# Optimization experiments

Hardware: AMD Instinct MI355X
Metric: run time of the kernel (lower is better)

## Reference

```python
import jax, jax.numpy as jnp
import numpy as np

B, C, S, D = 64, 729, 243, 512


def _layer_norm(x, gamma, beta, eps=1e-5):
    mu = jnp.mean(x, axis=-1, keepdims=True)
    var = jnp.mean((x - mu) ** 2, axis=-1, keepdims=True)
    return (x - mu) * jax.lax.rsqrt(var + eps) * gamma + beta


def setup_inputs() -> dict:
    key = jax.random.key(0)
    ks = jax.random.split(key, 8)
    s = 1.0 / np.sqrt(D)
    return {
        "cand_feat": jax.random.normal(ks[0], (B, C, D), dtype=jnp.float32),
        "set_feat": jax.random.normal(ks[1], (B, S, D), dtype=jnp.float32),
        "W_vc": jax.random.uniform(ks[2], (D, D), jnp.float32, -s, s),
        "b_vc": jnp.zeros((D,), jnp.float32),
        "W_vs": jax.random.uniform(ks[3], (D, D), jnp.float32, -s, s),
        "b_vs": jnp.zeros((D,), jnp.float32),
        "ff_W1": jax.random.uniform(ks[4], (2 * D, D), jnp.float32, -s, s),
        "ff_b1": jnp.zeros((2 * D,), jnp.float32),
        "ff_W2": jax.random.uniform(ks[5], (D, 2 * D), jnp.float32, -1.0 / np.sqrt(2 * D), 1.0 / np.sqrt(2 * D)),
        "ff_b2": jnp.zeros((D,), jnp.float32),
        "g_set": jnp.ones((D,), jnp.float32),
        "be_set": jnp.zeros((D,), jnp.float32),
        "g_cand": jnp.ones((D,), jnp.float32),
        "be_cand": jnp.zeros((D,), jnp.float32),
        "g_ff": jnp.ones((D,), jnp.float32),
        "be_ff": jnp.zeros((D,), jnp.float32),
        "cand_to_set_idx": jax.random.randint(ks[6], (C, 3), 0, S, dtype=jnp.int64 if jax.config.jax_enable_x64 else jnp.int32),
    }


def reference(cand_feat, set_feat, W_vc, b_vc, W_vs, b_vs, ff_W1, ff_b1, ff_W2, ff_b2,
              g_set, be_set, g_cand, be_cand, g_ff, be_ff, cand_to_set_idx):
    b, c, d = cand_feat.shape
    idx = cand_to_set_idx.reshape(-1)  # (2187,)

    cand_msgs = cand_feat @ W_vc.T + b_vc              # (B, 729, D)
    msgs3 = jnp.repeat(cand_msgs, 3, axis=1)           # (B, 2187, D)
    set_updates = jnp.zeros_like(set_feat).at[:, idx, :].add(msgs3) / 9.0
    set_out = _layer_norm(set_feat + set_updates, g_set, be_set)

    # set -> cand: gather 3 sets per candidate, mean, linear
    gathered = set_out[:, idx, :].reshape(b, c, 3, d)  # (B, 729, 3, D)
    cand_updates = gathered.mean(axis=2) @ W_vs.T + b_vs
    cand_h = _layer_norm(cand_feat + cand_updates, g_cand, be_cand)

    # FF block with residual
    ff = jax.nn.relu(cand_h @ ff_W1.T + ff_b1) @ ff_W2.T + ff_b2
    cand_out = _layer_norm(cand_h + ff, g_ff, be_ff)
    return (cand_out, set_out)
```

## Files before the change

### kernel.cpp

```cpp
#include <hip/hip_runtime.h>

using u16 = unsigned short;
using u32 = unsigned int;

typedef __attribute__((ext_vector_type(8))) short bf16x8;
typedef __attribute__((ext_vector_type(4))) float f32x4;
typedef __attribute__((ext_vector_type(8))) u16 u16x8;
typedef __attribute__((ext_vector_type(4))) u16 u16x4;

constexpr int NB = 64, NC = 729, NS = 243, ND = 512, ND2 = 1024;
constexpr int MS = NB * NS;
constexpr int MC = NB * NC;

__device__ __forceinline__ u16 f2bf(float f) {
  u32 u = __builtin_bit_cast(u32, f);
  return (u16)((u + 0x7fffu + ((u >> 16) & 1u)) >> 16);
}
__device__ __forceinline__ float bf2f(u16 h) {
  return __builtin_bit_cast(float, (u32)h << 16);
}
__device__ __forceinline__ void gload16(const void* g, void* l) {
  __builtin_amdgcn_global_load_lds((const __attribute__((address_space(1))) u32*)g,
                                   (__attribute__((address_space(3))) u32*)l, 16, 0, 0);
}

__global__ __launch_bounds__(256) void cast_all_k(const float* __restrict__ s0,
                                                  const float* __restrict__ s1,
                                                  const float* __restrict__ s2,
                                                  const float* __restrict__ s3,
                                                  u16* __restrict__ d0, u16* __restrict__ d1,
                                                  u16* __restrict__ d2, u16* __restrict__ d3) {
  int i = blockIdx.x * 256 + threadIdx.x;
  const float* s; u16* d; int off;
  if (i < 65536)       { s = s0; d = d0; off = i; }
  else if (i < 131072) { s = s1; d = d1; off = i - 65536; }
  else if (i < 262144) { s = s2; d = d2; off = i - 131072; }
  else                 { s = s3; d = d3; off = i - 262144; }
  f32x4 v = ((const f32x4*)s)[off];
  u16x4 o;
  o.x = f2bf(v.x); o.y = f2bf(v.y); o.z = f2bf(v.z); o.w = f2bf(v.w);
  ((u16x4*)d)[off] = o;
}

__global__ __launch_bounds__(1024) void build_csr_k(const int* __restrict__ idx,
                                                    int* __restrict__ offs,
                                                    int* __restrict__ list) {
  constexpr int NE = 3 * NC;
  constexpr int NCH = (NE + 63) / 64;
  __shared__ int sidx[NE];
  __shared__ int lrank[NE];
  __shared__ int hist[NCH][NS];
  __shared__ int scan[256];
  __shared__ int soffs[NS];
  const int t = threadIdx.x;
  const int wv = t >> 6, ln = t & 63;

  for (int e = t; e < NE; e += 1024) sidx[e] = idx[e];
  for (int i = t; i < NCH * NS; i += 1024) (&hist[0][0])[i] = 0;
  __syncthreads();

  for (int c = wv; c < NCH; c += 16) {
    int e = c * 64 + ln;
    int s = (e < NE) ? sidx[e] : -1;
    int rank = 0, tot = 0;
#pragma unroll
    for (int l2 = 0; l2 < 64; ++l2) {
      int v = __shfl(s, l2);
      bool m = (v == s) && (s >= 0);
      rank += (m && (l2 < ln)) ? 1 : 0;
      tot  += m ? 1 : 0;
    }
    if (e < NE) {
      lrank[e] = rank;
      if (rank == 0) hist[c][s] = tot;
    }
  }
  __syncthreads();

  int mycnt = 0;
  if (t < NS) {
    int run = 0;
#pragma unroll 5
    for (int c = 0; c < NCH; ++c) { int v = hist[c][t]; hist[c][t] = run; run += v; }
    mycnt = run;
  }
  if (t < 256) scan[t] = (t < NS) ? mycnt : 0;
  __syncthreads();

  for (int d = 1; d < 256; d <<= 1) {
    int v = 0;
    if (t < 256 && t >= d) v = scan[t - d];
    __syncthreads();
    if (t < 256) scan[t] += v;
    __syncthreads();
  }
  if (t < NS) {
    soffs[t] = scan[t] - mycnt;
    offs[t] = scan[t] - mycnt;
  }
  if (t == 0) offs[NS] = NE;
  __syncthreads();

  for (int e = t; e < NE; e += 1024) {
    int s = sidx[e];
    list[soffs[s] + hist[e >> 6][s] + lrank[e]] = e / 3;
  }
}

__global__ __launch_bounds__(256) void agg_k(const float* __restrict__ cand_feat,
                                             const int* __restrict__ offs,
                                             const int* __restrict__ list,
                                             u16* __restrict__ agg) {
  int row = blockIdx.x * 4 + (threadIdx.x >> 6);
  if (row >= MS) return;
  int lane = threadIdx.x & 63;
  int b = row / NS, s = row - b * NS;
  int e0 = offs[s], e1 = offs[s + 1];
  const float* base = cand_feat + (size_t)b * NC * ND + lane * 8;
  f32x4 a0 = {0.f, 0.f, 0.f, 0.f}, a1 = {0.f, 0.f, 0.f, 0.f};
  for (int e = e0; e < e1; ++e) {
    const float* p = base + (size_t)list[e] * ND;
    a0 += *(const f32x4*)p;
    a1 += *(const f32x4*)(p + 4);
  }
  u16x8 o;
  o[0] = f2bf(a0.x); o[1] = f2bf(a0.y); o[2] = f2bf(a0.z); o[3] = f2bf(a0.w);
  o[4] = f2bf(a1.x); o[5] = f2bf(a1.y); o[6] = f2bf(a1.z); o[7] = f2bf(a1.w);
  *(u16x8*)(agg + (size_t)row * ND + lane * 8) = o;
}

template <int EP>
__global__ __launch_bounds__(256, 4) void gemm_k64(const u16* __restrict__ A,
                                                   const u16* __restrict__ Bw,
                                                   void* __restrict__ Out,
                                                   const float* __restrict__ bias,
                                                   int M, int N, int K) {
  constexpr int BK = 64;
  __shared__ u16 lA[128 * BK];
  __shared__ u16 lB[128 * BK];
  const int t = threadIdx.x, wid = t >> 6, lane = t & 63;
  const int NT = N >> 7;
  const int nwg = gridDim.x;
  int wg;
  { int q = nwg >> 3, r = nwg & 7, x = blockIdx.x & 7, p = blockIdx.x >> 3;
    wg = (x < r ? x * (q + 1) : r * (q + 1) + (x - r) * q) + p; }
  const int mt = wg / NT, nt = wg % NT;
  const int m0 = mt << 7, n0 = nt << 7;

  const u16* gA[4]; const u16* gB[4]; int ldo[4];
#pragma unroll
  for (int i = 0; i < 4; ++i) {
    int s = i * 256 + t;
    int r = s >> 3, j = s & 7;
    int cj = (j ^ (r & 7)) * 8;
    int ar = m0 + r; if (ar > M - 1) ar = M - 1;
    gA[i] = A + (size_t)ar * K + cj;
    gB[i] = Bw + (size_t)(n0 + r) * K + cj;
    ldo[i] = s * 8;
  }

  const int li = lane & 15, g0 = lane >> 4;
  const int wr = wid >> 1, wc = wid & 1;
  int aOff[4], bOff[4];
#pragma unroll
  for (int i = 0; i < 4; ++i) {
    int rowA = wr * 64 + i * 16 + li;
    int rowB = wc * 64 + i * 16 + li;
    aOff[i] = rowA * 64 + ((g0 ^ (li & 7)) << 3);
    bOff[i] = rowB * 64 + ((g0 ^ (li & 7)) << 3);
  }

  f32x4 acc[4][4] = {};

  for (int kt = 0; kt < K; kt += BK) {
#pragma unroll
    for (int i = 0; i < 4; ++i) gload16(gA[i], lA + ldo[i]);
#pragma unroll
    for (int i = 0; i < 4; ++i) gload16(gB[i], lB + ldo[i]);
#pragma unroll
    for (int i = 0; i < 4; ++i) { gA[i] += BK; gB[i] += BK; }
    __syncthreads();
#pragma unroll
    for (int kk = 0; kk < 2; ++kk) {
      bf16x8 af[4], bfr[4];
#pragma unroll
      for (int i = 0; i < 4; ++i) {
        af[i]  = *(const bf16x8*)(lA + (aOff[i] ^ (kk << 5)));
        bfr[i] = *(const bf16x8*)(lB + (bOff[i] ^ (kk << 5)));
      }
#pragma unroll
      for (int mi = 0; mi < 4; ++mi)
#pragma unroll
        for (int ni = 0; ni < 4; ++ni)
          acc[mi][ni] = __builtin_amdgcn_mfma_f32_16x16x32_bf16(af[mi], bfr[ni], acc[mi][ni], 0, 0, 0);
    }
    __syncthreads();
  }

  const int rb = m0 + wr * 64 + (g0 << 2);
  const int cb = n0 + wc * 64 + li;
  if (EP == 0) {
    float* O = (float*)Out;
#pragma unroll
    for (int mi = 0; mi < 4; ++mi)
#pragma unroll
      for (int ni = 0; ni < 4; ++ni) {
        int cc = cb + ni * 16;
#pragma unroll
        for (int r = 0; r < 4; ++r) {
          int rr = rb + mi * 16 + r;
          if (rr < M) O[(size_t)rr * N + cc] = acc[mi][ni][r];
        }
      }
  } else {
    u16* O = (u16*)Out;
    float bv[4];
#pragma unroll
    for (int ni = 0; ni < 4; ++ni) bv[ni] = (EP == 3) ? 0.0f : bias[cb + ni * 16];
#pragma unroll
    for (int mi = 0; mi < 4; ++mi)
#pragma unroll
      for (int ni = 0; ni < 4; ++ni) {
        int cc = cb + ni * 16;
#pragma unroll
        for (int r = 0; r < 4; ++r) {
          int rr = rb + mi * 16 + r;
          float v = acc[mi][ni][r] + bv[ni];
          if (EP == 1) v = fmaxf(v, 0.0f);
          if (rr < M) O[(size_t)rr * N + cc] = f2bf(v);
        }
      }
  }
}

__global__ __launch_bounds__(256) void set_ln_k(const u16* __restrict__ u1,
                                                const float* __restrict__ set_feat,
                                                const int* __restrict__ offs,
                                                const float* __restrict__ b_vc,
                                                const float* __restrict__ gam,
                                                const float* __restrict__ bet,
                                                float* __restrict__ set_out,
                                                u16* __restrict__ set_out_bf) {
  int row = blockIdx.x * 4 + (threadIdx.x >> 6);
  if (row >= MS) return;
  int lane = threadIdx.x & 63;
  int s = row % NS;
  float c9 = (float)(offs[s + 1] - offs[s]) * (1.0f / 9.0f);
  size_t base = (size_t)row * ND + lane * 8;
  u16x8 ua = *(const u16x8*)(u1 + base);
  f32x4 s0 = *(const f32x4*)(set_feat + base), s1  = *(const f32x4*)(set_feat + base + 4);
  f32x4 b0 = *(const f32x4*)(b_vc + lane * 8), b1  = *(const f32x4*)(b_vc + lane * 8 + 4);
  f32x4 x0, x1;
#pragma unroll
  for (int i = 0; i < 4; ++i) {
    x0[i] = s0[i] + bf2f(ua[i]) * (1.0f / 9.0f) + b0[i] * c9;
    x1[i] = s1[i] + bf2f(ua[i + 4]) * (1.0f / 9.0f) + b1[i] * c9;
  }
  float sm = 0.f, sq = 0.f;
#pragma unroll
  for (int i = 0; i < 4; ++i) { sm += x0[i] + x1[i]; sq += x0[i] * x0[i] + x1[i] * x1[i]; }
#pragma unroll
  for (int m = 32; m; m >>= 1) { sm += __shfl_xor(sm, m); sq += __shfl_xor(sq, m); }
  float mu = sm * (1.0f / ND);
  float rs = rsqrtf(sq * (1.0f / ND) - mu * mu + 1e-5f);
  f32x4 g0 = *(const f32x4*)(gam + lane * 8), g1 = *(const f32x4*)(gam + lane * 8 + 4);
  f32x4 e0 = *(const f32x4*)(bet + lane * 8), e1 = *(const f32x4*)(bet + lane * 8 + 4);
  f32x4 y0, y1; u16x8 ob;
#pragma unroll
  for (int i = 0; i < 4; ++i) {
    y0[i] = (x0[i] - mu) * rs * g0[i] + e0[i];
    y1[i] = (x1[i] - mu) * rs * g1[i] + e1[i];
    ob[i] = f2bf(y0[i]); ob[i + 4] = f2bf(y1[i]);
  }
  *(f32x4*)(set_out + base) = y0;
  *(f32x4*)(set_out + base + 4) = y1;
  *(u16x8*)(set_out_bf + base) = ob;
}

__global__ __launch_bounds__(256) void cand_ln_k(const float* __restrict__ cand_feat,
                                                 const u16* __restrict__ proj,
                                                 const int* __restrict__ cidx,
                                                 const float* __restrict__ b_vs,
                                                 const float* __restrict__ gam,
                                                 const float* __restrict__ bet,
                                                 u16* __restrict__ cand_h) {
  int row = blockIdx.x * 4 + (threadIdx.x >> 6);
  if (row >= MC) return;
  int lane = threadIdx.x & 63;
  int b = row / NC, c = row - b * NC;
  int i0 = cidx[c * 3], i1 = cidx[c * 3 + 1], i2 = cidx[c * 3 + 2];
  const u16* pb = proj + (size_t)b * NS * ND + lane * 8;
  u16x8 p0 = *(const u16x8*)(pb + (size_t)i0 * ND);
  u16x8 p1 = *(const u16x8*)(pb + (size_t)i1 * ND);
  u16x8 p2 = *(const u16x8*)(pb + (size_t)i2 * ND);
  size_t base = (size_t)row * ND + lane * 8;
  f32x4 c0 = *(const f32x4*)(cand_feat + base), c1 = *(const f32x4*)(cand_feat + base + 4);
  f32x4 v0 = *(const f32x4*)(b_vs + lane * 8),  v1 = *(const f32x4*)(b_vs + lane * 8 + 4);
  const float third = 1.0f / 3.0f;
  f32x4 x0, x1;
#pragma unroll
  for (int i = 0; i < 4; ++i) {
    x0[i] = c0[i] + (bf2f(p0[i]) + bf2f(p1[i]) + bf2f(p2[i])) * third + v0[i];
    x1[i] = c1[i] + (bf2f(p0[i + 4]) + bf2f(p1[i + 4]) + bf2f(p2[i + 4])) * third + v1[i];
  }
  float sm = 0.f, sq = 0.f;
#pragma unroll
  for (int i = 0; i < 4; ++i) { sm += x0[i] + x1[i]; sq += x0[i] * x0[i] + x1[i] * x1[i]; }
#pragma unroll
  for (int m = 32; m; m >>= 1) { sm += __shfl_xor(sm, m); sq += __shfl_xor(sq, m); }
  float mu = sm * (1.0f / ND);
  float rs = rsqrtf(sq * (1.0f / ND) - mu * mu + 1e-5f);
  f32x4 g0 = *(const f32x4*)(gam + lane * 8), g1 = *(const f32x4*)(gam + lane * 8 + 4);
  f32x4 e0 = *(const f32x4*)(bet + lane * 8), e1 = *(const f32x4*)(bet + lane * 8 + 4);
  u16x8 ob;
#pragma unroll
  for (int i = 0; i < 4; ++i) {
    ob[i]     = f2bf((x0[i] - mu) * rs * g0[i] + e0[i]);
    ob[i + 4] = f2bf((x1[i] - mu) * rs * g1[i] + e1[i]);
  }
  *(u16x8*)(cand_h + base) = ob;
}

__global__ __launch_bounds__(256) void ln_ff_k(const u16* __restrict__ h2b,
                                               const u16* __restrict__ resid,
                                               const float* __restrict__ gam,
                                               const float* __restrict__ bet,
                                               float* __restrict__ out, int nrows) {
  int row = blockIdx.x * 4 + (threadIdx.x >> 6);
  if (row >= nrows) return;
  int lane = threadIdx.x & 63;
  size_t base = (size_t)row * ND + lane * 8;
  u16x8 ha = *(const u16x8*)(h2b + base);
  u16x8 ra = *(const u16x8*)(resid + base);
  float x[8];
  float sm = 0.f, sq = 0.f;
#pragma unroll
  for (int i = 0; i < 8; ++i) {
    x[i] = bf2f(ha[i]) + bf2f(ra[i]);
    sm += x[i]; sq += x[i] * x[i];
  }
#pragma unroll
  for (int m = 32; m; m >>= 1) { sm += __shfl_xor(sm, m); sq += __shfl_xor(sq, m); }
  float mu = sm * (1.0f / ND);
  float rs = rsqrtf(sq * (1.0f / ND) - mu * mu + 1e-5f);
  f32x4 g0 = *(const f32x4*)(gam + lane * 8), g1 = *(const f32x4*)(gam + lane * 8 + 4);
  f32x4 e0 = *(const f32x4*)(bet + lane * 8), e1 = *(const f32x4*)(bet + lane * 8 + 4);
  f32x4 y0, y1;
#pragma unroll
  for (int i = 0; i < 4; ++i) {
    y0[i] = (x[i] - mu) * rs * g0[i] + e0[i];
    y1[i] = (x[i + 4] - mu) * rs * g1[i] + e1[i];
  }
  *(f32x4*)(out + base) = y0;
  *(f32x4*)(out + base + 4) = y1;
}

extern "C" void kernel_launch(void* const* d_in, const int* in_sizes, int n_in,
                              void* d_out, int out_size, void* d_ws, size_t ws_size,
                              hipStream_t stream) {
  const float* cand_feat = (const float*)d_in[0];
  const float* set_feat  = (const float*)d_in[1];
  const float* W_vc  = (const float*)d_in[2];
  const float* b_vc  = (const float*)d_in[3];
  const float* W_vs  = (const float*)d_in[4];
  const float* b_vs  = (const float*)d_in[5];
  const float* ff_W1 = (const float*)d_in[6];
  const float* ff_b1 = (const float*)d_in[7];
  const float* ff_W2 = (const float*)d_in[8];
  const float* ff_b2 = (const float*)d_in[9];
  const float* g_set  = (const float*)d_in[10];
  const float* be_set = (const float*)d_in[11];
  const float* g_cand = (const float*)d_in[12];
  const float* be_cand= (const float*)d_in[13];
  const float* g_ff   = (const float*)d_in[14];
  const float* be_ff  = (const float*)d_in[15];
  const int*   cidx   = (const int*)d_in[16];
  (void)in_sizes; (void)n_in; (void)out_size; (void)ws_size;

  char* ws = (char*)d_ws;
  u16* w_vc_b = (u16*)(ws + 0);
  u16* w_vs_b = (u16*)(ws + (512 << 10));
  u16* w1_b   = (u16*)(ws + (1 << 20));
  u16* w2_b   = (u16*)(ws + (2 << 20));
  int* offs   = (int*)(ws + (3 << 20));
  int* list   = (int*)(ws + (3 << 20) + 4096);
  u16* setb   = (u16*)(ws + (4 << 20));
  u16* candh  = (u16*)(ws + (20 << 20));
  u16* h2b    = (u16*)(ws + (size_t)(68 << 20));

  float* out_cand = (float*)d_out;
  float* out_set  = out_cand + (size_t)MC * ND;
  u16*   agg  = (u16*)out_set;
  u16*   u1   = (u16*)out_cand;
  u16*   proj = (u16*)out_cand;
  u16*   h1   = (u16*)out_cand;

  cast_all_k<<<1536, 256, 0, stream>>>(W_vc, W_vs, ff_W1, ff_W2, w_vc_b, w_vs_b, w1_b, w2_b);
  build_csr_k<<<1, 1024, 0, stream>>>(cidx, offs, list);
  agg_k<<<(MS + 3) / 4, 256, 0, stream>>>(cand_feat, offs, list, agg);
  gemm_k64<3><<<122 * 4, 256, 0, stream>>>(agg, w_vc_b, u1, nullptr, MS, ND, ND);
  set_ln_k<<<(MS + 3) / 4, 256, 0, stream>>>(u1, set_feat, offs, b_vc, g_set, be_set, out_set, setb);
  gemm_k64<3><<<122 * 4, 256, 0, stream>>>(setb, w_vs_b, proj, nullptr, MS, ND, ND);
  cand_ln_k<<<(MC + 3) / 4, 256, 0, stream>>>(cand_feat, proj, cidx, b_vs, g_cand, be_cand, candh);
  gemm_k64<1><<<365 * 8, 256, 0, stream>>>(candh, w1_b, h1, ff_b1, MC, ND2, ND);
  gemm_k64<2><<<365 * 4, 256, 0, stream>>>(h1, w2_b, h2b, ff_b2, MC, ND, ND2);
  ln_ff_k<<<(MC + 3) / 4, 256, 0, stream>>>(h2b, candh, g_ff, be_ff, out_cand, MC);
}
```

Baseline: 312.8 us.

## Use double-buffered 256x256-tile GEMM for feed-forward layers

Adds a 512-thread GEMM kernel with 256x256 output tiles and two LDS buffers, so the load of the next K-slice overlaps the MFMA work on the current one. Both feed-forward GEMMs now use it, which gives each block more data reuse and cuts global and LDS traffic per FLOP. The small GEMM's epilogue is reduced to the plain bf16 store path, and the XCD swizzle is pulled into a helper. In exchange, the 128KB of LDS per block limits each CU to one block, and the second GEMM's grid fills the GPU poorly in its last wave.

```diff
diff --git a/kernel.cpp b/kernel.cpp
--- a/kernel.cpp
+++ b/kernel.cpp
@@ -22,6 +22,10 @@
 __device__ __forceinline__ void gload16(const void* g, void* l) {
   __builtin_amdgcn_global_load_lds((const __attribute__((address_space(1))) u32*)g,
                                    (__attribute__((address_space(3))) u32*)l, 16, 0, 0);
+}
+__device__ __forceinline__ int xcd_swz(int bid, int nwg) {
+  int q = nwg >> 3, r = nwg & 7, x = bid & 7, p = bid >> 3;
+  return (x < r ? x * (q + 1) : r * (q + 1) + (x - r) * q) + p;
 }
 
 __global__ __launch_bounds__(256) void cast_all_k(const float* __restrict__ s0,
@@ -140,10 +144,7 @@
   __shared__ u16 lB[128 * BK];
   const int t = threadIdx.x, wid = t >> 6, lane = t & 63;
   const int NT = N >> 7;
-  const int nwg = gridDim.x;
-  int wg;
-  { int q = nwg >> 3, r = nwg & 7, x = blockIdx.x & 7, p = blockIdx.x >> 3;
-    wg = (x < r ? x * (q + 1) : r * (q + 1) + (x - r) * q) + p; }
+  const int wg = xcd_swz(blockIdx.x, gridDim.x);
   const int mt = wg / NT, nt = wg % NT;
   const int m0 = mt << 7, n0 = nt << 7;
 
@@ -164,10 +165,8 @@
   int aOff[4], bOff[4];
 #pragma unroll
   for (int i = 0; i < 4; ++i) {
-    int rowA = wr * 64 + i * 16 + li;
-    int rowB = wc * 64 + i * 16 + li;
-    aOff[i] = rowA * 64 + ((g0 ^ (li & 7)) << 3);
-    bOff[i] = rowB * 64 + ((g0 ^ (li & 7)) << 3);
+    aOff[i] = (wr * 64 + i * 16 + li) * 64 + ((g0 ^ (li & 7)) << 3);
+    bOff[i] = (wc * 64 + i * 16 + li) * 64 + ((g0 ^ (li & 7)) << 3);
   }
 
   f32x4 acc[4][4] = {};
@@ -199,38 +198,120 @@
 
   const int rb = m0 + wr * 64 + (g0 << 2);
   const int cb = n0 + wc * 64 + li;
-  if (EP == 0) {
-    float* O = (float*)Out;
-#pragma unroll
-    for (int mi = 0; mi < 4; ++mi)
-#pragma unroll
-      for (int ni = 0; ni < 4; ++ni) {
-        int cc = cb + ni * 16;
-#pragma unroll
-        for (int r = 0; r < 4; ++r) {
-          int rr = rb + mi * 16 + r;
-          if (rr < M) O[(size_t)rr * N + cc] = acc[mi][ni][r];
-        }
+  u16* O = (u16*)Out;
+#pragma unroll
+  for (int mi = 0; mi < 4; ++mi)
+#pragma unroll
+    for (int ni = 0; ni < 4; ++ni) {
+      int cc = cb + ni * 16;
+#pragma unroll
+      for (int r = 0; r < 4; ++r) {
+        int rr = rb + mi * 16 + r;
+        float v = acc[mi][ni][r];
+        if (rr < M) O[(size_t)rr * N + cc] = f2bf(v);
       }
-  } else {
-    u16* O = (u16*)Out;
-    float bv[4];
-#pragma unroll
-    for (int ni = 0; ni < 4; ++ni) bv[ni] = (EP == 3) ? 0.0f : bias[cb + ni * 16];
-#pragma unroll
-    for (int mi = 0; mi < 4; ++mi)
-#pragma unroll
-      for (int ni = 0; ni < 4; ++ni) {
-        int cc = cb + ni * 16;
-#pragma unroll
-        for (int r = 0; r < 4; ++r) {
-          int rr = rb + mi * 16 + r;
-          float v = acc[mi][ni][r] + bv[ni];
-          if (EP == 1) v = fmaxf(v, 0.0f);
-          if (rr < M) O[(size_t)rr * N + cc] = f2bf(v);
-        }
+    }
+}
+
+template <int EP>
+__global__ __launch_bounds__(512) void gemm256_k(const u16* __restrict__ A,
+                                                 const u16* __restrict__ Bw,
+                                                 u16* __restrict__ Out,
+                                                 const float* __restrict__ bias,
+                                                 int M, int N, int K) {
+  constexpr int BK = 64;
+  __shared__ u16 lA0[256 * BK], lB0[256 * BK];
+  __shared__ u16 lA1[256 * BK], lB1[256 * BK];
+  const int t = threadIdx.x, wid = t >> 6, lane = t & 63;
+  const int NT = N >> 8;
+  const int wg = xcd_swz(blockIdx.x, gridDim.x);
+  const int mt = wg / NT, nt = wg % NT;
+  const int m0 = mt << 8, n0 = nt << 8;
+
+  const u16* gA[4]; const u16* gB[4]; int ldo[4];
+#pragma unroll
+  for (int i = 0; i < 4; ++i) {
+    int s = i * 512 + t;
+    int r = s >> 3, j = s & 7;
+    int cj = (j ^ (r & 7)) * 8;
+    int ar = m0 + r; if (ar > M - 1) ar = M - 1;
+    gA[i] = A + (size_t)ar * K + cj;
+    gB[i] = Bw + (size_t)(n0 + r) * K + cj;
+    ldo[i] = s * 8;
+  }
+
+  const int li = lane & 15, g0 = lane >> 4;
+  const int wr = wid >> 2, wc = wid & 3;
+  int aOff[8], bOff[4];
+#pragma unroll
+  for (int mi = 0; mi < 8; ++mi)
+    aOff[mi] = (wr * 128 + mi * 16 + li) * 64 + ((g0 ^ (li & 7)) << 3);
+#pragma unroll
+  for (int ni = 0; ni < 4; ++ni)
+    bOff[ni] = (wc * 64 + ni * 16 + li) * 64 + ((g0 ^ (li & 7)) << 3);
+
+  f32x4 acc[8][4] = {};
+  const int nk = K / BK;
+
+  auto STAGE = [&](u16* dA, u16* dB) {
+#pragma unroll
+    for (int i = 0; i < 4; ++i) gload16(gA[i], dA + ldo[i]);
+#pragma unroll
+    for (int i = 0; i < 4; ++i) gload16(gB[i], dB + ldo[i]);
+#pragma unroll
+    for (int i = 0; i < 4; ++i) { gA[i] += BK; gB[i] += BK; }
+  };
+  auto COMPUTE = [&](const u16* cA, const u16* cB) {
+#pragma unroll
+    for (int kk = 0; kk < 2; ++kk) {
+      bf16x8 bfr[4];
+#pragma unroll
+      for (int ni = 0; ni < 4; ++ni) bfr[ni] = *(const bf16x8*)(cB + (bOff[ni] ^ (kk << 5)));
+#pragma unroll
+      for (int mh = 0; mh < 2; ++mh) {
+        bf16x8 af[4];
+#pragma unroll
+        for (int q = 0; q < 4; ++q) af[q] = *(const bf16x8*)(cA + (aOff[mh * 4 + q] ^ (kk << 5)));
+#pragma unroll
+        for (int q = 0; q < 4; ++q)
+#pragma unroll
+          for (int ni = 0; ni < 4; ++ni)
+            acc[mh * 4 + q][ni] =
+                __builtin_amdgcn_mfma_f32_16x16x32_bf16(af[q], bfr[ni], acc[mh * 4 + q][ni], 0, 0, 0);
       }
-  }
+    }
+  };
+
+  STAGE(lA0, lB0);
+  __syncthreads();
+#pragma unroll 1
+  for (int ks = 0; ks < nk; ks += 2) {
+    STAGE(lA1, lB1);
+    COMPUTE(lA0, lB0);
+    __syncthreads();
+    if (ks + 2 < nk) STAGE(lA0, lB0);
+    COMPUTE(lA1, lB1);
+    __syncthreads();
+  }
+
+  const int rb = m0 + wr * 128 + (g0 << 2);
+  const int cb = n0 + wc * 64 + li;
+  float bv[4];
+#pragma unroll
+  for (int ni = 0; ni < 4; ++ni) bv[ni] = bias[cb + ni * 16];
+#pragma unroll
+  for (int mi = 0; mi < 8; ++mi)
+#pragma unroll
+    for (int ni = 0; ni < 4; ++ni) {
+      int cc = cb + ni * 16;
+#pragma unroll
+      for (int r = 0; r < 4; ++r) {
+        int rr = rb + mi * 16 + r;
+        float v = acc[mi][ni][r] + bv[ni];
+        if (EP == 1) v = fmaxf(v, 0.0f);
+        if (rr < M) Out[(size_t)rr * N + cc] = f2bf(v);
+      }
+    }
 }
 
 __global__ __launch_bounds__(256) void set_ln_k(const u16* __restrict__ u1,
@@ -402,7 +483,7 @@
   set_ln_k<<<(MS + 3) / 4, 256, 0, stream>>>(u1, set_feat, offs, b_vc, g_set, be_set, out_set, setb);
   gemm_k64<3><<<122 * 4, 256, 0, stream>>>(setb, w_vs_b, proj, nullptr, MS, ND, ND);
   cand_ln_k<<<(MC + 3) / 4, 256, 0, stream>>>(cand_feat, proj, cidx, b_vs, g_cand, be_cand, candh);
-  gemm_k64<1><<<365 * 8, 256, 0, stream>>>(candh, w1_b, h1, ff_b1, MC, ND2, ND);
-  gemm_k64<2><<<365 * 4, 256, 0, stream>>>(h1, w2_b, h2b, ff_b2, MC, ND, ND2);
+  gemm256_k<1><<<183 * 4, 512, 0, stream>>>(candh, w1_b, h1, ff_b1, MC, ND2, ND);
+  gemm256_k<2><<<183 * 2, 512, 0, stream>>>(h1, w2_b, h2b, ff_b2, MC, ND, ND2);
   ln_ff_k<<<(MC + 3) / 4, 256, 0, stream>>>(h2b, candh, g_ff, be_ff, out_cand, MC);
 }
```

Result: slower. 341.3 us (+9.1%).
